# Optimization experiments

Hardware: AMD Instinct MI355X
Metric: run time of the kernel (lower is better)

Reference implementation:

```python
import jax, jax.numpy as jnp
import numpy as np

HIDDEN = 4096
KERNEL = 4
BATCH = 4096


def setup_inputs() -> dict:
    key = jax.random.key(0)
    k1, k2, k3, k4 = jax.random.split(key, 4)
    x = jax.random.normal(k1, (BATCH, HIDDEN), dtype=jnp.float32)
    state = jax.random.normal(k2, (BATCH, HIDDEN, KERNEL - 1), dtype=jnp.float32)
    # depthwise Conv1d(H, H, K, groups=H): weight [H, 1, K] -> stored as [H, K]
    fan_in = KERNEL  # per-group in_channels(=1) * kernel_size
    bound = 1.0 / np.sqrt(fan_in)
    weight = jax.random.uniform(k3, (HIDDEN, KERNEL), minval=-bound, maxval=bound, dtype=jnp.float32)
    bias = jax.random.uniform(k4, (HIDDEN,), minval=-bound, maxval=bound, dtype=jnp.float32)
    return {"x": x, "state": state, "weight": weight, "bias": bias}


def reference(x, state, weight, bias):
    # x: [B, H], state: [B, H, K-1]
    x_with_state = jnp.concatenate([state, x[:, :, None]], axis=-1)  # [B, H, K]
    # depthwise conv over a length-K window -> single output step per channel
    out = jnp.einsum('bhk,hk->bh', x_with_state, weight) + bias  # [B, H]
    new_state = x_with_state[:, :, 1:]  # [B, H, K-1]
    return out, new_state
```

## Files before the change

### kernel.cpp

```cpp
#include <hip/hip_runtime.h>


#ifndef CC_HIDDEN
#define CC_HIDDEN 4096
#endif
#ifndef CC_BATCH
#define CC_BATCH 4096
#endif

__global__ __launch_bounds__(256) void causal_conv1d_kernel(
    const float* __restrict__ x,
    const float* __restrict__ state,
    const float* __restrict__ weight,
    const float* __restrict__ bias,
    float* __restrict__ out,
    float* __restrict__ new_state)
{
    const long long g = (long long)blockIdx.x * blockDim.x + threadIdx.x;
    const long long ngroups = (long long)CC_BATCH * CC_HIDDEN / 4;
    if (g >= ngroups) return;

    const int hq = (int)(g % (CC_HIDDEN / 4));
    const int h0 = hq * 4;
    const long long base = g * 4;

    const float4 xv = *reinterpret_cast<const float4*>(x + base);
    const float4* sp = reinterpret_cast<const float4*>(state + base * 3);
    const float4 s0 = sp[0];
    const float4 s1 = sp[1];
    const float4 s2 = sp[2];
    const float4* wp = reinterpret_cast<const float4*>(weight + (long long)h0 * 4);
    const float4 w0 = wp[0], w1 = wp[1], w2 = wp[2], w3 = wp[3];
    const float4 bv = *reinterpret_cast<const float4*>(bias + h0);

    float4 o;
    o.x = fmaf(s0.x, w0.x, fmaf(s0.y, w0.y, fmaf(s0.z, w0.z, fmaf(xv.x, w0.w, bv.x))));
    o.y = fmaf(s0.w, w1.x, fmaf(s1.x, w1.y, fmaf(s1.y, w1.z, fmaf(xv.y, w1.w, bv.y))));
    o.z = fmaf(s1.z, w2.x, fmaf(s1.w, w2.y, fmaf(s2.x, w2.z, fmaf(xv.z, w2.w, bv.z))));
    o.w = fmaf(s2.y, w3.x, fmaf(s2.z, w3.y, fmaf(s2.w, w3.z, fmaf(xv.w, w3.w, bv.w))));
    *reinterpret_cast<float4*>(out + base) = o;

    float4 n0, n1, n2;
    n0.x = s0.y; n0.y = s0.z; n0.z = xv.x; n0.w = s1.x;
    n1.x = s1.y; n1.y = xv.y; n1.z = s1.w; n1.w = s2.x;
    n2.x = xv.z; n2.y = s2.z; n2.z = s2.w; n2.w = xv.w;
    float4* np = reinterpret_cast<float4*>(new_state + base * 3);
    np[0] = n0; np[1] = n1; np[2] = n2;
}

extern "C" void kernel_launch(void* const* d_in, const int* in_sizes, int n_in,
                              void* d_out, int out_size, void* d_ws, size_t ws_size,
                              hipStream_t stream) {
    const float* x      = (const float*)d_in[0];
    const float* state  = (const float*)d_in[1];
    const float* weight = (const float*)d_in[2];
    const float* bias   = (const float*)d_in[3];

    const long long BH = (long long)CC_BATCH * CC_HIDDEN;
    float* out       = (float*)d_out;
    float* new_state = (float*)d_out + BH;

    const long long ngroups = BH / 4;
    const int block = 256;
    const int grid = (int)((ngroups + block - 1) / block);

    causal_conv1d_kernel<<<grid, block, 0, stream>>>(x, state, weight, bias, out, new_state);
}
```

Measured before the change: 444.0 us.

## Stage state loads and stores through LDS for fully coalesced float4 access

State reads and new_state writes now go through shared memory. Each thread loads and stores consecutive float4s across the block, so a warp touches one contiguous span instead of the 48-byte per-thread stride used before. Compute reads the transposed planes from LDS, which is padded to avoid bank conflicts. This adds two block barriers and LDS traffic to a kernel that is purely memory-bound.

```diff
diff --git a/kernel.cpp b/kernel.cpp
--- a/kernel.cpp
+++ b/kernel.cpp
@@ -1,14 +1,13 @@
 #include <hip/hip_runtime.h>
 
 
-#ifndef CC_HIDDEN
-#define CC_HIDDEN 4096
-#endif
-#ifndef CC_BATCH
-#define CC_BATCH 4096
-#endif
+#define CC_H 4096
+#define CC_B 4096
+#define BLOCK 256
+#define EPB (BLOCK * 4)
+#define PLANE 257
 
-__global__ __launch_bounds__(256) void causal_conv1d_kernel(
+__global__ __launch_bounds__(BLOCK) void causal_conv1d_kernel(
     const float* __restrict__ x,
     const float* __restrict__ state,
     const float* __restrict__ weight,
@@ -16,36 +15,62 @@
     float* __restrict__ out,
     float* __restrict__ new_state)
 {
-    const long long g = (long long)blockIdx.x * blockDim.x + threadIdx.x;
-    const long long ngroups = (long long)CC_BATCH * CC_HIDDEN / 4;
-    if (g >= ngroups) return;
+    __shared__ float4 lds[3 * PLANE];
 
-    const int hq = (int)(g % (CC_HIDDEN / 4));
-    const int h0 = hq * 4;
-    const long long base = g * 4;
+    const int tid = threadIdx.x;
+    const long long base_e  = (long long)blockIdx.x * EPB;
+    const long long base_x4 = base_e >> 2;
+    const long long base_s4 = (base_e * 3) >> 2;
 
-    const float4 xv = *reinterpret_cast<const float4*>(x + base);
-    const float4* sp = reinterpret_cast<const float4*>(state + base * 3);
-    const float4 s0 = sp[0];
-    const float4 s1 = sp[1];
-    const float4 s2 = sp[2];
+    const float4* stateF4 = reinterpret_cast<const float4*>(state);
+    const float4* xF4     = reinterpret_cast<const float4*>(x);
+
+    #pragma unroll
+    for (int i = 0; i < 3; ++i) {
+        const int j = i * BLOCK + tid;
+        const int t = j / 3;
+        const int s = j - t * 3;
+        lds[s * PLANE + t] = stateF4[base_s4 + j];
+    }
+
+    const int h0 = (int)(base_e & (CC_H - 1)) + tid * 4;
     const float4* wp = reinterpret_cast<const float4*>(weight + (long long)h0 * 4);
     const float4 w0 = wp[0], w1 = wp[1], w2 = wp[2], w3 = wp[3];
     const float4 bv = *reinterpret_cast<const float4*>(bias + h0);
+    const float4 xv = xF4[base_x4 + tid];
+
+    __syncthreads();
+
+    const float4 s0 = lds[0 * PLANE + tid];
+    const float4 s1 = lds[1 * PLANE + tid];
+    const float4 s2 = lds[2 * PLANE + tid];
 
     float4 o;
     o.x = fmaf(s0.x, w0.x, fmaf(s0.y, w0.y, fmaf(s0.z, w0.z, fmaf(xv.x, w0.w, bv.x))));
     o.y = fmaf(s0.w, w1.x, fmaf(s1.x, w1.y, fmaf(s1.y, w1.z, fmaf(xv.y, w1.w, bv.y))));
     o.z = fmaf(s1.z, w2.x, fmaf(s1.w, w2.y, fmaf(s2.x, w2.z, fmaf(xv.z, w2.w, bv.z))));
     o.w = fmaf(s2.y, w3.x, fmaf(s2.z, w3.y, fmaf(s2.w, w3.z, fmaf(xv.w, w3.w, bv.w))));
-    *reinterpret_cast<float4*>(out + base) = o;
+    reinterpret_cast<float4*>(out)[base_x4 + tid] = o;
 
     float4 n0, n1, n2;
     n0.x = s0.y; n0.y = s0.z; n0.z = xv.x; n0.w = s1.x;
     n1.x = s1.y; n1.y = xv.y; n1.z = s1.w; n1.w = s2.x;
     n2.x = xv.z; n2.y = s2.z; n2.z = s2.w; n2.w = xv.w;
-    float4* np = reinterpret_cast<float4*>(new_state + base * 3);
-    np[0] = n0; np[1] = n1; np[2] = n2;
+
+    lds[0 * PLANE + tid] = n0;
+    lds[1 * PLANE + tid] = n1;
+    lds[2 * PLANE + tid] = n2;
+
+    __syncthreads();
+
+    float4* nsF4 = reinterpret_cast<float4*>(new_state);
+    #pragma unroll
+    for (int i = 0; i < 3; ++i) {
+        const int j = i * BLOCK + tid;
+        const int t = j / 3;
+        const int s = j - t * 3;
+        nsF4[base_s4 + j] = lds[s * PLANE + t];
+    }
 }
 
 extern "C" void kernel_launch(void* const* d_in, const int* in_sizes, int n_in,
@@ -56,13 +81,10 @@
     const float* weight = (const float*)d_in[2];
     const float* bias   = (const float*)d_in[3];
 
-    const long long BH = (long long)CC_BATCH * CC_HIDDEN;
+    const long long BH = (long long)CC_B * CC_H;
     float* out       = (float*)d_out;
     float* new_state = (float*)d_out + BH;
 
-    const long long ngroups = BH / 4;
-    const int block = 256;
-    const int grid = (int)((ngroups + block - 1) / block);
-
-    causal_conv1d_kernel<<<grid, block, 0, stream>>>(x, state, weight, bias, out, new_state);
+    const int grid = (int)(BH / EPB);
+    causal_conv1d_kernel<<<grid, BLOCK, 0, stream>>>(x, state, weight, bias, out, new_state);
 }
```

Result: faster. 430.0 us (-3.1%).
